# Kernel optimization log

Measured on AMD Instinct MI355X. Metric: run time of the kernel, lower is better.

Reference implementation:

```python
import jax, jax.numpy as jnp
import numpy as np

B, NA, NB = 2, 2048, 2048
DIM_A, DIM_B = 256, 256
HEADS, DH_A, DH_B = 8, 64, 64
INNER_A, INNER_B = DH_A * HEADS, DH_B * HEADS
EPS = 1e-5


def layer_norm(x, w, b):
    m = jnp.mean(x, axis=-1, keepdims=True)
    v = jnp.mean(jnp.square(x - m), axis=-1, keepdims=True)
    return (x - m) * jax.lax.rsqrt(v + EPS) * w + b


def setup_inputs() -> dict:
    key = jax.random.key(0)
    ks = jax.random.split(key, 16)
    s = 0.02
    return {
        "feat_a": jax.random.normal(ks[0], (B, NA, DIM_A), jnp.float32),
        "feat_b": jax.random.normal(ks[1], (B, NB, DIM_B), jnp.float32),
        "mask_a_b": jax.random.bernoulli(ks[2], 0.5, (B, NA, NB)),
        # linear weights stored (in, out)
        "Wq": jax.random.normal(ks[3], (DIM_A, INNER_B), jnp.float32) * s,
        "bq": jnp.zeros((INNER_B,), jnp.float32),
        "Wk": jax.random.normal(ks[4], (DIM_B, INNER_B), jnp.float32) * s,
        "bk": jnp.zeros((INNER_B,), jnp.float32),
        "Wv": jax.random.normal(ks[5], (DIM_B, INNER_A), jnp.float32) * s,
        "bv": jnp.zeros((INNER_A,), jnp.float32),
        "Wg": jax.random.normal(ks[6], (DIM_A, INNER_A), jnp.float32) * s,
        "bg": jnp.zeros((INNER_A,), jnp.float32),
        "Wo": jax.random.normal(ks[7], (INNER_A, DIM_A), jnp.float32) * s,
        "bo": jnp.zeros((DIM_A,), jnp.float32),
        "ln_a_w": jnp.ones((DIM_A,), jnp.float32),
        "ln_a_b": jnp.zeros((DIM_A,), jnp.float32),
        "ln_b_w": jnp.ones((DIM_B,), jnp.float32),
        "ln_b_b": jnp.zeros((DIM_B,), jnp.float32),
        "qln_w": jnp.ones((INNER_B,), jnp.float32),
        "qln_b": jnp.zeros((INNER_B,), jnp.float32),
        "kln_w": jnp.ones((INNER_B,), jnp.float32),
        "kln_b": jnp.zeros((INNER_B,), jnp.float32),
    }


def reference(feat_a, feat_b, mask_a_b, Wq, bq, Wk, bk, Wv, bv, Wg, bg, Wo, bo,
              ln_a_w, ln_a_b, ln_b_w, ln_b_b, qln_w, qln_b, kln_w, kln_b):
    scale = DH_B ** -0.5
    fa = layer_norm(feat_a, ln_a_w, ln_a_b)            # (b, na, dim_a)
    fb = layer_norm(feat_b, ln_b_w, ln_b_b)            # (b, nb, dim_b)
    q = layer_norm(fa @ Wq + bq, qln_w, qln_b)         # (b, na, inner_b)
    k = layer_norm(fb @ Wk + bk, kln_w, kln_b)         # (b, nb, inner_b)
    v = fb @ Wv + bv                                   # (b, nb, inner_a)
    g = fa @ Wg + bg                                   # (b, na, inner_a)
    q = q.reshape(B, NA, HEADS, DH_B)
    k = k.reshape(B, NB, HEADS, DH_B)
    v = v.reshape(B, NB, HEADS, DH_A)
    g = g.reshape(B, NA, HEADS, DH_A)
    sim = jnp.einsum('bihd,bjhd->bhij', q, k) * scale  # (b, h, na, nb)
    neg = jnp.finfo(sim.dtype).min
    sim = jnp.where(mask_a_b[:, None, :, :], sim, neg)
    attn = jax.nn.softmax(sim, axis=-1)
    out = jnp.einsum('bhij,bjhd->bihd', attn, v)       # (b, na, h, dh_a)
    out = jax.nn.sigmoid(g) * out
    out = out.reshape(B, NA, INNER_A)
    return out @ Wo + bo                               # (b, na, dim_a)
```

## Files before the change

kernel.cpp:

```cpp
#include <hip/hip_runtime.h>
#include <hip/hip_bf16.h>

using bf16 = __hip_bfloat16;
typedef short bf16x8 __attribute__((ext_vector_type(8)));
typedef float f32x4 __attribute__((ext_vector_type(4)));
typedef unsigned short ushort8_t __attribute__((ext_vector_type(8)));
typedef unsigned uint4_t __attribute__((ext_vector_type(4)));
typedef unsigned long long u64;

static constexpr int NA_ = 2048, NB_ = 2048;
static constexpr int H_ = 8, DH_ = 64, INNER_ = 512;
static constexpr int MROWS = 2 * NA_;

#define MFMA32(a, b, c) __builtin_amdgcn_mfma_f32_16x16x32_bf16(a, b, c, 0, 0, 0)

#if __has_builtin(__builtin_amdgcn_exp2f)
#define EXP2(x) __builtin_amdgcn_exp2f(x)
#else
#define EXP2(x) exp2f(x)
#endif

__device__ __forceinline__ unsigned short bfbits(float x) {
  bf16 h = __float2bfloat16(x);
  return __builtin_bit_cast(unsigned short, h);
}
__device__ __forceinline__ float b2f(unsigned short u) {
  unsigned v = ((unsigned)u) << 16;
  return __builtin_bit_cast(float, v);
}

__device__ __forceinline__ unsigned pkbf(float a, float b) {
  unsigned ua = __builtin_bit_cast(unsigned, a) + 0x8000u;
  unsigned ub = __builtin_bit_cast(unsigned, b) + 0x8000u;
#if __has_builtin(__builtin_amdgcn_perm)
  return __builtin_amdgcn_perm(ub, ua, 0x07060302u);
#else
  return (ua >> 16) | (ub & 0xFFFF0000u);
#endif
}

__global__ __launch_bounds__(256) void prep_kernel(
    const float* __restrict__ fa_in, const float* __restrict__ fb_in,
    const float* __restrict__ law, const float* __restrict__ lab,
    const float* __restrict__ lbw, const float* __restrict__ lbb,
    bf16* __restrict__ fa, bf16* __restrict__ fb,
    const float* __restrict__ Wq, const float* __restrict__ Wk,
    const float* __restrict__ Wv, const float* __restrict__ Wg,
    const float* __restrict__ Wo,
    bf16* __restrict__ Wqt, bf16* __restrict__ Wkt,
    bf16* __restrict__ Wvt, bf16* __restrict__ Wgt,
    bf16* __restrict__ Woth, bf16* __restrict__ Wotl,
    const void* __restrict__ maskp, u64* __restrict__ mbits) {
  int blk = blockIdx.x;
  int t = threadIdx.x;
  if (blk < 2048) {
    int row = blk * 4 + (t >> 6);
    int lane = t & 63;
    const float *src, *w, *bb;
    bf16* dst;
    int r;
    if (row < MROWS) { src = fa_in; w = law; bb = lab; dst = fa; r = row; }
    else             { src = fb_in; w = lbw; bb = lbb; dst = fb; r = row - MROWS; }
    float4 x = *(const float4*)(src + (size_t)r * 256 + lane * 4);
    float s  = (x.x + x.y) + (x.z + x.w);
    float s2 = (x.x * x.x + x.y * x.y) + (x.z * x.z + x.w * x.w);
#pragma unroll
    for (int m = 32; m >= 1; m >>= 1) { s += __shfl_xor(s, m); s2 += __shfl_xor(s2, m); }
    float mean = s * (1.0f / 256.0f);
    float var  = s2 * (1.0f / 256.0f) - mean * mean;
    float rstd = rsqrtf(var + 1e-5f);
    float4 wv = *(const float4*)(w + lane * 4);
    float4 bv = *(const float4*)(bb + lane * 4);
    ushort4 o;
    o.x = bfbits((x.x - mean) * rstd * wv.x + bv.x);
    o.y = bfbits((x.y - mean) * rstd * wv.y + bv.y);
    o.z = bfbits((x.z - mean) * rstd * wv.z + bv.z);
    o.w = bfbits((x.w - mean) * rstd * wv.w + bv.w);
    *(ushort4*)(dst + (size_t)r * 256 + lane * 4) = o;
  } else if (blk < 4608) {
    int z = (blk - 2048) >> 9;
    int idx = ((blk - 2048) & 511) * 256 + t;
    if (z < 4) {
      const float* W = (z == 0) ? Wq : (z == 1) ? Wk : (z == 2) ? Wv : Wg;
      bf16* Wt = (z == 0) ? Wqt : (z == 1) ? Wkt : (z == 2) ? Wvt : Wgt;
      int kk = idx >> 9, n = idx & 511;
      Wt[n * 256 + kk] = __float2bfloat16(W[idx]);
    } else {
      int kk = idx >> 8, n = idx & 255;
      float w = Wo[idx];
      bf16 hi = __float2bfloat16(w);
      Woth[n * 512 + kk] = hi;
      Wotl[n * 512 + kk] = __float2bfloat16(w - __bfloat162float(hi));
    }
  } else {
    __shared__ unsigned shf[4];
    const unsigned char* mu = (const unsigned char*)maskp;
    bool nz = ((t & 3) != 0) && (mu[t] != 0);
    u64 bal = __ballot(nz);
    if ((t & 63) == 0) shf[t >> 6] = (bal != 0ull) ? 1u : 0u;
    __syncthreads();
    bool m8 = (shf[0] | shf[1] | shf[2] | shf[3]) != 0;
    int lane = t & 63, wid = t >> 6;
    int lb = blk - 4608;
    for (size_t word = (size_t)lb * 4 + wid; word < 131072; word += 8192) {
      size_t e = word * 64 + lane;
      int v = m8 ? (int)mu[e] : ((const int*)maskp)[e];
      u64 b2 = __ballot(v != 0);
      if (lane == 0) mbits[word] = b2;
    }
  }
}

__global__ __launch_bounds__(256) void gemm4_kernel(
    const bf16* __restrict__ fa, const bf16* __restrict__ fb,
    const bf16* __restrict__ Wqt, const bf16* __restrict__ Wkt,
    const bf16* __restrict__ Wgt, const bf16* __restrict__ Wvt,
    const float* __restrict__ bq, const float* __restrict__ bk,
    const float* __restrict__ bg, const float* __restrict__ bv,
    const float* __restrict__ qlw, const float* __restrict__ qlb,
    const float* __restrict__ klw, const float* __restrict__ klb,
    bf16* __restrict__ qo, bf16* __restrict__ ko,
    bf16* __restrict__ gout, bf16* __restrict__ vout) {
  __shared__ __align__(16) char sm[27648];
  int z = blockIdx.z;
  int t = threadIdx.x, wave = t >> 6, lane = t & 63;
  int lm = lane & 15, quad = lane >> 4, q8 = quad * 8;

  if (z < 2) {
    bf16* As = (bf16*)sm;
    float* Pred = (float*)(sm + 16896);
    float* MV   = (float*)(sm + 17408);
    const bf16* A    = z ? fb : fa;
    const bf16* Wt   = z ? Wkt : Wqt;
    const float* bias = z ? bk : bq;
    const float* lw  = z ? klw : qlw;
    const float* lb  = z ? klb : qlb;
    bf16* out        = z ? ko : qo;
    int m0 = blockIdx.x * 16;
#pragma unroll
    for (int i = 0; i < 2; i++) {
      int id = t + 256 * i, r = id >> 5, cg = id & 31;
      *(ushort8_t*)(&As[r * 264 + cg * 8]) =
          *(const ushort8_t*)(A + (size_t)(m0 + r) * 256 + cg * 8);
    }
    __syncthreads();
    int n0w = wave * 128;
    f32x4 acc[8] = {};
    const bf16* wrow[8];
#pragma unroll
    for (int ni = 0; ni < 8; ni++) wrow[ni] = Wt + (size_t)(n0w + ni * 16 + lm) * 256;
#pragma unroll
    for (int ks = 0; ks < 8; ks++) {
      int k0 = ks * 32;
      bf16x8 af = *(const bf16x8*)(&As[lm * 264 + k0 + q8]);
#pragma unroll
      for (int ni = 0; ni < 8; ni++) {
        bf16x8 bf_ = *(const bf16x8*)(wrow[ni] + k0 + q8);
        acc[ni] = MFMA32(af, bf_, acc[ni]);
      }
    }
    float bvv[8];
#pragma unroll
    for (int ni = 0; ni < 8; ni++) bvv[ni] = bias[n0w + ni * 16 + lm];
#pragma unroll
    for (int ni = 0; ni < 8; ni++)
#pragma unroll
      for (int r = 0; r < 4; r++) acc[ni][r] += bvv[ni];
#pragma unroll
    for (int r = 0; r < 4; r++) {
      float s = 0.f, s2 = 0.f;
#pragma unroll
      for (int ni = 0; ni < 8; ni++) { s += acc[ni][r]; s2 += acc[ni][r] * acc[ni][r]; }
#pragma unroll
      for (int m = 1; m <= 8; m <<= 1) { s += __shfl_xor(s, m); s2 += __shfl_xor(s2, m); }
      if (lm == 0) {
        int row = quad * 4 + r;
        Pred[row * 8 + wave * 2]     = s;
        Pred[row * 8 + wave * 2 + 1] = s2;
      }
    }
    __syncthreads();
    if (t < 16) {
      float s = 0.f, s2 = 0.f;
#pragma unroll
      for (int w = 0; w < 4; w++) { s += Pred[t * 8 + w * 2]; s2 += Pred[t * 8 + w * 2 + 1]; }
      float mean = s * (1.0f / 512.0f);
      float var  = s2 * (1.0f / 512.0f) - mean * mean;
      MV[t * 2]     = mean;
      MV[t * 2 + 1] = rsqrtf(var + 1e-5f);
    }
    __syncthreads();
    float lww[8], lbb_[8];
#pragma unroll
    for (int ni = 0; ni < 8; ni++) {
      lww[ni]  = lw[n0w + ni * 16 + lm];
      lbb_[ni] = lb[n0w + ni * 16 + lm];
    }
    if (z == 0) {
      const float SC = 0.125f * 1.44269504088896f;
#pragma unroll
      for (int ni = 0; ni < 8; ni++) { lww[ni] *= SC; lbb_[ni] *= SC; }
    }
#pragma unroll
    for (int r = 0; r < 4; r++) {
      int row = quad * 4 + r;
      float mean = MV[row * 2], rstd = MV[row * 2 + 1];
      size_t obase = (size_t)(m0 + row) * 512 + n0w;
#pragma unroll
      for (int ni = 0; ni < 8; ni++)
        out[obase + ni * 16 + lm] =
            __float2bfloat16((acc[ni][r] - mean) * rstd * lww[ni] + lbb_[ni]);
    }
  } else {
    bf16* As = (bf16*)sm;
    bf16* Bs = (bf16*)(sm + 18432);
    const bf16* A    = (z == 3) ? fb : fa;
    const bf16* Wt   = (z == 3) ? Wvt : Wgt;
    const float* bias = (z == 3) ? bv : bg;
    int x = blockIdx.x;
    int m0 = (x >> 3) * 128, n0 = (x & 7) * 64;
    int wm = wave * 32;
    f32x4 acc[2][4] = {};
    for (int k0 = 0; k0 < 256; k0 += 64) {
      __syncthreads();
#pragma unroll
      for (int i = 0; i < 4; i++) {
        int id = t + 256 * i, r = id >> 3, cg = id & 7;
        *(ushort8_t*)(&As[r * 72 + cg * 8]) =
            *(const ushort8_t*)(A + (size_t)(m0 + r) * 256 + k0 + cg * 8);
      }
#pragma unroll
      for (int i = 0; i < 2; i++) {
        int id = t + 256 * i, r = id >> 3, cg = id & 7;
        *(ushort8_t*)(&Bs[r * 72 + cg * 8]) =
            *(const ushort8_t*)(Wt + (size_t)(n0 + r) * 256 + k0 + cg * 8);
      }
      __syncthreads();
#pragma unroll
      for (int kk = 0; kk < 64; kk += 32) {
        bf16x8 af[2], bf_[4];
#pragma unroll
        for (int mi = 0; mi < 2; mi++)
          af[mi] = *(const bf16x8*)(&As[(wm + mi * 16 + lm) * 72 + kk + q8]);
#pragma unroll
        for (int ni = 0; ni < 4; ni++)
          bf_[ni] = *(const bf16x8*)(&Bs[(ni * 16 + lm) * 72 + kk + q8]);
#pragma unroll
        for (int mi = 0; mi < 2; mi++)
#pragma unroll
          for (int ni = 0; ni < 4; ni++)
            acc[mi][ni] = MFMA32(af[mi], bf_[ni], acc[mi][ni]);
      }
    }
    if (z == 2) {
#pragma unroll
      for (int mi = 0; mi < 2; mi++)
#pragma unroll
        for (int ni = 0; ni < 4; ni++) {
          int nn = n0 + ni * 16 + lm;
          float bvv = bias[nn];
          int mb = m0 + wm + mi * 16 + quad * 4;
#pragma unroll
          for (int r = 0; r < 4; r++)
            gout[(size_t)(mb + r) * 512 + nn] = __float2bfloat16(acc[mi][ni][r] + bvv);
        }
    } else {
      __syncthreads();
      bf16* buf = (bf16*)sm;
#pragma unroll
      for (int mi = 0; mi < 2; mi++)
#pragma unroll
        for (int ni = 0; ni < 4; ni++) {
          int d_local = ni * 16 + lm;
          float bvv = bias[n0 + d_local];
          int j_local = wm + mi * 16 + quad * 4;
#pragma unroll
          for (int r = 0; r < 4; r++)
            buf[d_local * 136 + j_local + r] = __float2bfloat16(acc[mi][ni][r] + bvv);
        }
      __syncthreads();
      int bidx2 = m0 >> 11, j0g = m0 & 2047, hh = n0 >> 6;
      int dl = t >> 2, jseg = (t & 3) * 32;
      bf16* dstrow = vout + (size_t)((bidx2 * 8 + hh) * 64 + dl) * 2048 + j0g + jseg;
#pragma unroll
      for (int c = 0; c < 4; c++)
        *(ushort8_t*)(dstrow + c * 8) = *(const ushort8_t*)(&buf[dl * 136 + jseg + c * 8]);
    }
  }
}

__global__ __launch_bounds__(512, 6) void attn_kernel(
    const bf16* __restrict__ q, const bf16* __restrict__ k,
    const bf16* __restrict__ vt, const bf16* __restrict__ g,
    const u64* __restrict__ mbits,
    bf16* __restrict__ gh, bf16* __restrict__ gl) {
  __shared__ __align__(16) char smem[46592];
  bf16* Qs = (bf16*)smem;
  bf16* KsB = (bf16*)(smem + 9216);
  bf16* VsB = (bf16*)(smem + 27648);
  float* Om = (float*)(smem + 9216);
  float* Lbuf = (float*)(smem + 46080);

  int qt = blockIdx.x, bh = blockIdx.y;
  int bidx = bh >> 3, h = bh & 7;
  int i0 = qt * 64;
  int t = threadIdx.x, wave = t >> 6, lane = t & 63;
  int jhalf = wave >> 2, w4 = wave & 3;
  int lm = lane & 15, quad = lane >> 4, q8 = quad * 8;
  int lt = t & 255;
  int sr0 = lt >> 3, scg = (lt & 7) * 8;

  int ksrow = ((sr0 & 4) << 2) | ((sr0 & 24) >> 1) | (sr0 & 3);
  int ksl0 = ksrow * 72 + scg;
  int ksl1 = (ksrow + 32) * 72 + scg;
  int vsl0 = sr0 * 72 + scg;
  int vsl1 = (sr0 + 32) * 72 + scg;

  {
    int r = t >> 3, cg = t & 7;
    *(ushort8_t*)(&Qs[r * 72 + cg * 8]) =
        *(const ushort8_t*)(q + (size_t)(bidx * NA_ + i0 + r) * INNER_ + h * DH_ + cg * 8);
  }
  __syncthreads();
  bf16x8 bq0 = *(const bf16x8*)(&Qs[(w4 * 16 + lm) * 72 + q8]);
  bf16x8 bq1 = *(const bf16x8*)(&Qs[(w4 * 16 + lm) * 72 + 32 + q8]);

  bf16x8 bone;
  {
    short onev = (lm == 0) ? (short)0x3F80 : (short)0;
#pragma unroll
    for (int i = 0; i < 8; i++) bone[i] = onev;
  }

  f32x4 oacc[4] = {};
  f32x4 lacc = {};

  const bf16* kb = k + (size_t)(bidx * NB_) * INNER_ + h * DH_;
  const bf16* vb = vt + (size_t)(bh * DH_) * NB_;
  bf16* Ks = KsB + jhalf * (64 * 72);
  bf16* Vs = VsB + jhalf * (64 * 72);
  const u64* mrp = mbits + ((size_t)(bidx * NA_ + i0 + w4 * 16 + lm)) * (NB_ / 64) + jhalf * 16;

  const bf16* ksrc0 = kb + (size_t)(jhalf * 1024 + sr0) * INNER_ + scg;
  const bf16* ksrc1 = kb + (size_t)(jhalf * 1024 + sr0 + 32) * INNER_ + scg;
  const bf16* vsrc0 = vb + (size_t)sr0 * NB_ + jhalf * 1024 + scg;
  const bf16* vsrc1 = vb + (size_t)(sr0 + 32) * NB_ + jhalf * 1024 + scg;

  ushort8_t kr0, kr1, vr0, vr1;
  kr0 = *(const ushort8_t*)(ksrc0);
  kr1 = *(const ushort8_t*)(ksrc1);
  vr0 = *(const ushort8_t*)(vsrc0);
  vr1 = *(const ushort8_t*)(vsrc1);
  u64 smw = mrp[0] >> (quad * 8);

  for (int it = 0; it < 16; it++) {
    __syncthreads();
    *(ushort8_t*)(&Ks[ksl0]) = kr0;
    *(ushort8_t*)(&Ks[ksl1]) = kr1;
    *(ushort8_t*)(&Vs[vsl0]) = vr0;
    *(ushort8_t*)(&Vs[vsl1]) = vr1;
    __syncthreads();

    u64 nsm = smw;
    if (it < 15) {
      int joff = (it + 1) * 64;
      kr0 = *(const ushort8_t*)(ksrc0 + (size_t)joff * INNER_);
      kr1 = *(const ushort8_t*)(ksrc1 + (size_t)joff * INNER_);
      vr0 = *(const ushort8_t*)(vsrc0 + joff);
      vr1 = *(const ushort8_t*)(vsrc1 + joff);
      nsm = mrp[it + 1] >> (quad * 8);
    }

    f32x4 st[4];
#pragma unroll
    for (int nt = 0; nt < 4; nt++) {
      bf16x8 a0 = *(const bf16x8*)(&Ks[(nt * 16 + lm) * 72 + q8]);
      bf16x8 a1 = *(const bf16x8*)(&Ks[(nt * 16 + lm) * 72 + 32 + q8]);
      f32x4 a = {0.f, 0.f, 0.f, 0.f};
      a = MFMA32(a0, bq0, a);
      a = MFMA32(a1, bq1, a);
      st[nt] = a;
    }

    float pr[4][4];
#pragma unroll
    for (int nt = 0; nt < 4; nt++)
#pragma unroll
      for (int r = 0; r < 4; r++) {
        int bitix = (nt >> 1) * 32 + (nt & 1) * 4 + r;
        bool live = (smw >> bitix) & 1ull;
        float sv = live ? st[nt][r] : -200.0f;
        pr[nt][r] = EXP2(sv);
      }

    uint4_t ua, ub;
    ua[0] = pkbf(pr[0][0], pr[0][1]);
    ua[1] = pkbf(pr[0][2], pr[0][3]);
    ua[2] = pkbf(pr[1][0], pr[1][1]);
    ua[3] = pkbf(pr[1][2], pr[1][3]);
    ub[0] = pkbf(pr[2][0], pr[2][1]);
    ub[1] = pkbf(pr[2][2], pr[2][3]);
    ub[2] = pkbf(pr[3][0], pr[3][1]);
    ub[3] = pkbf(pr[3][2], pr[3][3]);
    bf16x8 ap0 = __builtin_bit_cast(bf16x8, ua);
    bf16x8 ap1 = __builtin_bit_cast(bf16x8, ub);

#pragma unroll
    for (int c = 0; c < 4; c++) {
      bf16x8 v0 = *(const bf16x8*)(&Vs[(c * 16 + lm) * 72 + q8]);
      bf16x8 v1 = *(const bf16x8*)(&Vs[(c * 16 + lm) * 72 + 32 + q8]);
      oacc[c] = MFMA32(ap0, v0, oacc[c]);
      oacc[c] = MFMA32(ap1, v1, oacc[c]);
    }
    lacc = MFMA32(ap0, bone, lacc);
    lacc = MFMA32(ap1, bone, lacc);

    smw = nsm;
  }

  __syncthreads();
  if (lm == 0) {
#pragma unroll
    for (int r = 0; r < 4; r++)
      Lbuf[jhalf * 64 + w4 * 16 + quad * 4 + r] = lacc[r];
  }
  if (jhalf == 1) {
#pragma unroll
    for (int c = 0; c < 4; c++)
#pragma unroll
      for (int r = 0; r < 4; r++)
        Om[w4 * (16 * 66) + (quad * 4 + r) * 66 + c * 16 + lm] = oacc[c][r];
  }
  __syncthreads();
  if (jhalf == 0) {
    int mrow = i0 + w4 * 16 + quad * 4;
    float inv[4];
#pragma unroll
    for (int r = 0; r < 4; r++) {
      float l = Lbuf[w4 * 16 + quad * 4 + r] + Lbuf[64 + w4 * 16 + quad * 4 + r];
      inv[r] = 1.0f / l;
    }
#pragma unroll
    for (int c = 0; c < 4; c++) {
      int col = h * DH_ + c * 16 + lm;
#pragma unroll
      for (int r = 0; r < 4; r++) {
        float o = oacc[c][r] + Om[w4 * (16 * 66) + (quad * 4 + r) * 66 + c * 16 + lm];
        size_t idx = (size_t)(bidx * NA_ + mrow + r) * INNER_ + col;
        float gv = b2f(__builtin_bit_cast(unsigned short, g[idx]));
        float sig = 1.0f / (1.0f + __expf(-gv));
        float val = o * inv[r] * sig;
        unsigned short hb = bfbits(val);
        gh[idx] = __builtin_bit_cast(bf16, hb);
        gl[idx] = __float2bfloat16(val - b2f(hb));
      }
    }
  }
}

__global__ __launch_bounds__(256) void gemm_split_kernel(
    const bf16* __restrict__ Ah, const bf16* __restrict__ Al,
    const bf16* __restrict__ Bh, const bf16* __restrict__ Bl,
    const float* __restrict__ bias, float* __restrict__ C) {
  constexpr int K = 512, N = 256;
  __shared__ __align__(16) bf16 Ash[32 * 72];
  __shared__ __align__(16) bf16 Asl[32 * 72];
  __shared__ __align__(16) bf16 Bsh[64 * 72];
  __shared__ __align__(16) bf16 Bsl[64 * 72];
  int n0 = blockIdx.x * 64, m0 = blockIdx.y * 32;
  int t = threadIdx.x, wave = t >> 6, lane = t & 63;
  int lm = lane & 15, quad = lane >> 4, q8 = quad * 8;
  int wm = (wave & 1) * 16, wn = (wave >> 1) * 32;
  f32x4 acc[2] = {};
  for (int k0 = 0; k0 < K; k0 += 64) {
    __syncthreads();
    {
      int r = t >> 3, cg = t & 7;
      size_t ga = (size_t)(m0 + r) * K + k0 + cg * 8;
      *(ushort8_t*)(&Ash[r * 72 + cg * 8]) = *(const ushort8_t*)(Ah + ga);
      *(ushort8_t*)(&Asl[r * 72 + cg * 8]) = *(const ushort8_t*)(Al + ga);
    }
#pragma unroll
    for (int i = 0; i < 2; i++) {
      int id = t + 256 * i, r = id >> 3, cg = id & 7;
      size_t gb = (size_t)(n0 + r) * K + k0 + cg * 8;
      *(ushort8_t*)(&Bsh[r * 72 + cg * 8]) = *(const ushort8_t*)(Bh + gb);
      *(ushort8_t*)(&Bsl[r * 72 + cg * 8]) = *(const ushort8_t*)(Bl + gb);
    }
    __syncthreads();
#pragma unroll
    for (int kk = 0; kk < 64; kk += 32) {
      bf16x8 ah = *(const bf16x8*)(&Ash[(wm + lm) * 72 + kk + q8]);
      bf16x8 al = *(const bf16x8*)(&Asl[(wm + lm) * 72 + kk + q8]);
#pragma unroll
      for (int ni = 0; ni < 2; ni++) {
        bf16x8 bh_ = *(const bf16x8*)(&Bsh[(wn + ni * 16 + lm) * 72 + kk + q8]);
        bf16x8 bl_ = *(const bf16x8*)(&Bsl[(wn + ni * 16 + lm) * 72 + kk + q8]);
        acc[ni] = MFMA32(ah, bh_, acc[ni]);
        acc[ni] = MFMA32(ah, bl_, acc[ni]);
        acc[ni] = MFMA32(al, bh_, acc[ni]);
      }
    }
  }
#pragma unroll
  for (int ni = 0; ni < 2; ni++) {
    int n = n0 + wn + ni * 16 + lm;
    float bvv = bias[n];
    int mb = m0 + wm + quad * 4;
#pragma unroll
    for (int r = 0; r < 4; r++) C[(size_t)(mb + r) * N + n] = acc[ni][r] + bvv;
  }
}

extern "C" void kernel_launch(void* const* d_in, const int* in_sizes, int n_in,
                              void* d_out, int out_size, void* d_ws, size_t ws_size,
                              hipStream_t stream) {
  const float* feat_a = (const float*)d_in[0];
  const float* feat_b = (const float*)d_in[1];
  const void*  mask   = d_in[2];
  const float* Wq = (const float*)d_in[3];
  const float* bq = (const float*)d_in[4];
  const float* Wk = (const float*)d_in[5];
  const float* bk = (const float*)d_in[6];
  const float* Wv = (const float*)d_in[7];
  const float* bv = (const float*)d_in[8];
  const float* Wg = (const float*)d_in[9];
  const float* bg = (const float*)d_in[10];
  const float* Wo = (const float*)d_in[11];
  const float* bo = (const float*)d_in[12];
  const float* law = (const float*)d_in[13];
  const float* lab = (const float*)d_in[14];
  const float* lbw = (const float*)d_in[15];
  const float* lbb = (const float*)d_in[16];
  const float* qlw = (const float*)d_in[17];
  const float* qlb = (const float*)d_in[18];
  const float* klw = (const float*)d_in[19];
  const float* klb = (const float*)d_in[20];

  char* ws = (char*)d_ws;
  size_t off = 0;
  auto alloc = [&](size_t bytes) -> void* {
    void* p = ws + off;
    off += (bytes + 255) & ~(size_t)255;
    return p;
  };
  bf16* fa    = (bf16*)alloc((size_t)MROWS * 256 * 2);
  bf16* fb    = (bf16*)alloc((size_t)MROWS * 256 * 2);
  bf16* Wqt   = (bf16*)alloc((size_t)131072 * 2);
  bf16* Wkt   = (bf16*)alloc((size_t)131072 * 2);
  bf16* Wvt   = (bf16*)alloc((size_t)131072 * 2);
  bf16* Wgt   = (bf16*)alloc((size_t)131072 * 2);
  bf16* Woth  = (bf16*)alloc((size_t)131072 * 2);
  bf16* Wotl  = (bf16*)alloc((size_t)131072 * 2);
  bf16* qb_   = (bf16*)alloc((size_t)MROWS * 512 * 2);
  bf16* kb_   = (bf16*)alloc((size_t)MROWS * 512 * 2);
  bf16* vtb   = (bf16*)alloc((size_t)1024 * 2048 * 2);
  bf16* gbuf  = (bf16*)alloc((size_t)MROWS * 512 * 2);
  bf16* gh    = (bf16*)alloc((size_t)MROWS * 512 * 2);
  bf16* gl    = (bf16*)alloc((size_t)MROWS * 512 * 2);
  u64*  mbits = (u64*)alloc((size_t)131072 * 8);

  prep_kernel<<<6656, 256, 0, stream>>>(
      feat_a, feat_b, law, lab, lbw, lbb, fa, fb,
      Wq, Wk, Wv, Wg, Wo, Wqt, Wkt, Wvt, Wgt, Woth, Wotl, mask, mbits);
  gemm4_kernel<<<dim3(256, 1, 4), 256, 0, stream>>>(
      fa, fb, Wqt, Wkt, Wgt, Wvt, bq, bk, bg, bv,
      qlw, qlb, klw, klb, qb_, kb_, gbuf, vtb);
  attn_kernel<<<dim3(32, 16), 512, 0, stream>>>(qb_, kb_, vtb, gbuf, mbits, gh, gl);
  gemm_split_kernel<<<dim3(4, 128), 256, 0, stream>>>(gh, gl, Woth, Wotl, bo, (float*)d_out);
}
```

Baseline: 195.1 us.

## Retile attention waves into 2x2 query/key sub-blocks with four-way partial reduction

Each wave now computes a 32x32 query-by-key score tile instead of a 16x64 strip, so every K fragment is reused across two query row groups and every V fragment read from shared memory feeds two accumulators. This cuts LDS reads per MFMA. In exchange each wave holds twice the output accumulators and per-row sums, so the launch bound drops from 6 to 4 waves per SIMD. The epilogue becomes a four-way reduction through shared memory with extra barriers, and the Lbuf region grows to hold four partial row sums.

```diff
diff --git a/kernel.cpp b/kernel.cpp
--- a/kernel.cpp
+++ b/kernel.cpp
@@ -289,12 +289,12 @@
   }
 }
 
-__global__ __launch_bounds__(512, 6) void attn_kernel(
+__global__ __launch_bounds__(512, 4) void attn_kernel(
     const bf16* __restrict__ q, const bf16* __restrict__ k,
     const bf16* __restrict__ vt, const bf16* __restrict__ g,
     const u64* __restrict__ mbits,
     bf16* __restrict__ gh, bf16* __restrict__ gl) {
-  __shared__ __align__(16) char smem[46592];
+  __shared__ __align__(16) char smem[47104];
   bf16* Qs = (bf16*)smem;
   bf16* KsB = (bf16*)(smem + 9216);
   bf16* VsB = (bf16*)(smem + 27648);
@@ -305,8 +305,9 @@
   int bidx = bh >> 3, h = bh & 7;
   int i0 = qt * 64;
   int t = threadIdx.x, wave = t >> 6, lane = t & 63;
-  int jhalf = wave >> 2, w4 = wave & 3;
+  int jh = wave >> 2, wj = (wave >> 1) & 1, wi = wave & 1;
   int lm = lane & 15, quad = lane >> 4, q8 = quad * 8;
+  int wj32 = wj * 32, wi32 = wi * 32;
   int lt = t & 255;
   int sr0 = lt >> 3, scg = (lt & 7) * 8;
 
@@ -322,8 +323,10 @@
         *(const ushort8_t*)(q + (size_t)(bidx * NA_ + i0 + r) * INNER_ + h * DH_ + cg * 8);
   }
   __syncthreads();
-  bf16x8 bq0 = *(const bf16x8*)(&Qs[(w4 * 16 + lm) * 72 + q8]);
-  bf16x8 bq1 = *(const bf16x8*)(&Qs[(w4 * 16 + lm) * 72 + 32 + q8]);
+  bf16x8 bq00 = *(const bf16x8*)(&Qs[(wi32 + lm) * 72 + q8]);
+  bf16x8 bq01 = *(const bf16x8*)(&Qs[(wi32 + lm) * 72 + 32 + q8]);
+  bf16x8 bq10 = *(const bf16x8*)(&Qs[(wi32 + 16 + lm) * 72 + q8]);
+  bf16x8 bq11 = *(const bf16x8*)(&Qs[(wi32 + 16 + lm) * 72 + 32 + q8]);
 
   bf16x8 bone;
   {
@@ -332,26 +335,29 @@
     for (int i = 0; i < 8; i++) bone[i] = onev;
   }
 
-  f32x4 oacc[4] = {};
-  f32x4 lacc = {};
+  f32x4 oacc[2][4] = {};
+  f32x4 lacc[2] = {};
 
   const bf16* kb = k + (size_t)(bidx * NB_) * INNER_ + h * DH_;
   const bf16* vb = vt + (size_t)(bh * DH_) * NB_;
-  bf16* Ks = KsB + jhalf * (64 * 72);
-  bf16* Vs = VsB + jhalf * (64 * 72);
-  const u64* mrp = mbits + ((size_t)(bidx * NA_ + i0 + w4 * 16 + lm)) * (NB_ / 64) + jhalf * 16;
-
-  const bf16* ksrc0 = kb + (size_t)(jhalf * 1024 + sr0) * INNER_ + scg;
-  const bf16* ksrc1 = kb + (size_t)(jhalf * 1024 + sr0 + 32) * INNER_ + scg;
-  const bf16* vsrc0 = vb + (size_t)sr0 * NB_ + jhalf * 1024 + scg;
-  const bf16* vsrc1 = vb + (size_t)(sr0 + 32) * NB_ + jhalf * 1024 + scg;
+  bf16* Ks = KsB + jh * (64 * 72);
+  bf16* Vs = VsB + jh * (64 * 72);
+  const u64* mrp0 = mbits + ((size_t)(bidx * NA_ + i0 + wi32 + lm)) * (NB_ / 64) + jh * 16;
+  const u64* mrp1 = mrp0 + 16 * (NB_ / 64);
+  int shp = wj32 + quad * 8;
+
+  const bf16* ksrc0 = kb + (size_t)(jh * 1024 + sr0) * INNER_ + scg;
+  const bf16* ksrc1 = kb + (size_t)(jh * 1024 + sr0 + 32) * INNER_ + scg;
+  const bf16* vsrc0 = vb + (size_t)sr0 * NB_ + jh * 1024 + scg;
+  const bf16* vsrc1 = vb + (size_t)(sr0 + 32) * NB_ + jh * 1024 + scg;
 
   ushort8_t kr0, kr1, vr0, vr1;
   kr0 = *(const ushort8_t*)(ksrc0);
   kr1 = *(const ushort8_t*)(ksrc1);
   vr0 = *(const ushort8_t*)(vsrc0);
   vr1 = *(const ushort8_t*)(vsrc1);
-  u64 smw = mrp[0] >> (quad * 8);
+  u64 smw0 = mrp0[0] >> shp;
+  u64 smw1 = mrp1[0] >> shp;
 
   for (int it = 0; it < 16; it++) {
     __syncthreads();
@@ -361,98 +367,135 @@
     *(ushort8_t*)(&Vs[vsl1]) = vr1;
     __syncthreads();
 
-    u64 nsm = smw;
+    u64 n0m = smw0, n1m = smw1;
     if (it < 15) {
       int joff = (it + 1) * 64;
       kr0 = *(const ushort8_t*)(ksrc0 + (size_t)joff * INNER_);
       kr1 = *(const ushort8_t*)(ksrc1 + (size_t)joff * INNER_);
       vr0 = *(const ushort8_t*)(vsrc0 + joff);
       vr1 = *(const ushort8_t*)(vsrc1 + joff);
-      nsm = mrp[it + 1] >> (quad * 8);
-    }
-
-    f32x4 st[4];
-#pragma unroll
-    for (int nt = 0; nt < 4; nt++) {
-      bf16x8 a0 = *(const bf16x8*)(&Ks[(nt * 16 + lm) * 72 + q8]);
-      bf16x8 a1 = *(const bf16x8*)(&Ks[(nt * 16 + lm) * 72 + 32 + q8]);
-      f32x4 a = {0.f, 0.f, 0.f, 0.f};
-      a = MFMA32(a0, bq0, a);
-      a = MFMA32(a1, bq1, a);
-      st[nt] = a;
-    }
-
-    float pr[4][4];
-#pragma unroll
-    for (int nt = 0; nt < 4; nt++)
-#pragma unroll
-      for (int r = 0; r < 4; r++) {
-        int bitix = (nt >> 1) * 32 + (nt & 1) * 4 + r;
-        bool live = (smw >> bitix) & 1ull;
-        float sv = live ? st[nt][r] : -200.0f;
-        pr[nt][r] = EXP2(sv);
-      }
-
-    uint4_t ua, ub;
-    ua[0] = pkbf(pr[0][0], pr[0][1]);
-    ua[1] = pkbf(pr[0][2], pr[0][3]);
-    ua[2] = pkbf(pr[1][0], pr[1][1]);
-    ua[3] = pkbf(pr[1][2], pr[1][3]);
-    ub[0] = pkbf(pr[2][0], pr[2][1]);
-    ub[1] = pkbf(pr[2][2], pr[2][3]);
-    ub[2] = pkbf(pr[3][0], pr[3][1]);
-    ub[3] = pkbf(pr[3][2], pr[3][3]);
-    bf16x8 ap0 = __builtin_bit_cast(bf16x8, ua);
-    bf16x8 ap1 = __builtin_bit_cast(bf16x8, ub);
+      n0m = mrp0[it + 1] >> shp;
+      n1m = mrp1[it + 1] >> shp;
+    }
+
+    bf16x8 a00 = *(const bf16x8*)(&Ks[(wj32 + lm) * 72 + q8]);
+    bf16x8 a01 = *(const bf16x8*)(&Ks[(wj32 + lm) * 72 + 32 + q8]);
+    bf16x8 a10 = *(const bf16x8*)(&Ks[(wj32 + 16 + lm) * 72 + q8]);
+    bf16x8 a11 = *(const bf16x8*)(&Ks[(wj32 + 16 + lm) * 72 + 32 + q8]);
+    f32x4 st[2][2];
+    {
+      f32x4 x;
+      x = f32x4{0.f, 0.f, 0.f, 0.f};
+      x = MFMA32(a00, bq00, x); x = MFMA32(a01, bq01, x); st[0][0] = x;
+      x = f32x4{0.f, 0.f, 0.f, 0.f};
+      x = MFMA32(a10, bq00, x); x = MFMA32(a11, bq01, x); st[0][1] = x;
+      x = f32x4{0.f, 0.f, 0.f, 0.f};
+      x = MFMA32(a00, bq10, x); x = MFMA32(a01, bq11, x); st[1][0] = x;
+      x = f32x4{0.f, 0.f, 0.f, 0.f};
+      x = MFMA32(a10, bq10, x); x = MFMA32(a11, bq11, x); st[1][1] = x;
+    }
+
+#pragma unroll
+    for (int is_ = 0; is_ < 2; is_++) {
+      u64 w = is_ ? smw1 : smw0;
+#pragma unroll
+      for (int js = 0; js < 2; js++)
+#pragma unroll
+        for (int r = 0; r < 4; r++) {
+          bool live = (w >> (js * 4 + r)) & 1ull;
+          float sv = live ? st[is_][js][r] : -200.0f;
+          st[is_][js][r] = EXP2(sv);
+        }
+    }
+
+    uint4_t u0, u1;
+    u0[0] = pkbf(st[0][0][0], st[0][0][1]);
+    u0[1] = pkbf(st[0][0][2], st[0][0][3]);
+    u0[2] = pkbf(st[0][1][0], st[0][1][1]);
+    u0[3] = pkbf(st[0][1][2], st[0][1][3]);
+    u1[0] = pkbf(st[1][0][0], st[1][0][1]);
+    u1[1] = pkbf(st[1][0][2], st[1][0][3]);
+    u1[2] = pkbf(st[1][1][0], st[1][1][1]);
+    u1[3] = pkbf(st[1][1][2], st[1][1][3]);
+    bf16x8 pa0 = __builtin_bit_cast(bf16x8, u0);
+    bf16x8 pa1 = __builtin_bit_cast(bf16x8, u1);
 
 #pragma unroll
     for (int c = 0; c < 4; c++) {
-      bf16x8 v0 = *(const bf16x8*)(&Vs[(c * 16 + lm) * 72 + q8]);
-      bf16x8 v1 = *(const bf16x8*)(&Vs[(c * 16 + lm) * 72 + 32 + q8]);
-      oacc[c] = MFMA32(ap0, v0, oacc[c]);
-      oacc[c] = MFMA32(ap1, v1, oacc[c]);
-    }
-    lacc = MFMA32(ap0, bone, lacc);
-    lacc = MFMA32(ap1, bone, lacc);
-
-    smw = nsm;
+      bf16x8 v_ = *(const bf16x8*)(&Vs[(c * 16 + lm) * 72 + wj32 + q8]);
+      oacc[0][c] = MFMA32(pa0, v_, oacc[0][c]);
+      oacc[1][c] = MFMA32(pa1, v_, oacc[1][c]);
+    }
+    lacc[0] = MFMA32(pa0, bone, lacc[0]);
+    lacc[1] = MFMA32(pa1, bone, lacc[1]);
+
+    smw0 = n0m;
+    smw1 = n1m;
   }
 
   __syncthreads();
   if (lm == 0) {
 #pragma unroll
-    for (int r = 0; r < 4; r++)
-      Lbuf[jhalf * 64 + w4 * 16 + quad * 4 + r] = lacc[r];
-  }
-  if (jhalf == 1) {
-#pragma unroll
-    for (int c = 0; c < 4; c++)
+    for (int is_ = 0; is_ < 2; is_++)
 #pragma unroll
       for (int r = 0; r < 4; r++)
-        Om[w4 * (16 * 66) + (quad * 4 + r) * 66 + c * 16 + lm] = oacc[c][r];
+        Lbuf[(jh * 2 + wj) * 64 + wi32 + is_ * 16 + quad * 4 + r] = lacc[is_][r];
+  }
+  if (jh == 1 && wj == 1) {
+#pragma unroll
+    for (int is_ = 0; is_ < 2; is_++)
+#pragma unroll
+      for (int c = 0; c < 4; c++)
+#pragma unroll
+        for (int r = 0; r < 4; r++)
+          Om[(wi32 + is_ * 16 + quad * 4 + r) * 66 + c * 16 + lm] = oacc[is_][c][r];
   }
   __syncthreads();
-  if (jhalf == 0) {
-    int mrow = i0 + w4 * 16 + quad * 4;
-    float inv[4];
-#pragma unroll
-    for (int r = 0; r < 4; r++) {
-      float l = Lbuf[w4 * 16 + quad * 4 + r] + Lbuf[64 + w4 * 16 + quad * 4 + r];
-      inv[r] = 1.0f / l;
-    }
-#pragma unroll
-    for (int c = 0; c < 4; c++) {
-      int col = h * DH_ + c * 16 + lm;
+  if (jh == 1 && wj == 0) {
+#pragma unroll
+    for (int is_ = 0; is_ < 2; is_++)
+#pragma unroll
+      for (int c = 0; c < 4; c++)
+#pragma unroll
+        for (int r = 0; r < 4; r++)
+          Om[(wi32 + is_ * 16 + quad * 4 + r) * 66 + c * 16 + lm] += oacc[is_][c][r];
+  }
+  __syncthreads();
+  if (jh == 0 && wj == 1) {
+#pragma unroll
+    for (int is_ = 0; is_ < 2; is_++)
+#pragma unroll
+      for (int c = 0; c < 4; c++)
+#pragma unroll
+        for (int r = 0; r < 4; r++)
+          Om[(wi32 + is_ * 16 + quad * 4 + r) * 66 + c * 16 + lm] += oacc[is_][c][r];
+  }
+  __syncthreads();
+  if (jh == 0 && wj == 0) {
+#pragma unroll
+    for (int is_ = 0; is_ < 2; is_++) {
+      int ib = wi32 + is_ * 16 + quad * 4;
+      float inv[4];
 #pragma unroll
       for (int r = 0; r < 4; r++) {
-        float o = oacc[c][r] + Om[w4 * (16 * 66) + (quad * 4 + r) * 66 + c * 16 + lm];
-        size_t idx = (size_t)(bidx * NA_ + mrow + r) * INNER_ + col;
-        float gv = b2f(__builtin_bit_cast(unsigned short, g[idx]));
-        float sig = 1.0f / (1.0f + __expf(-gv));
-        float val = o * inv[r] * sig;
-        unsigned short hb = bfbits(val);
-        gh[idx] = __builtin_bit_cast(bf16, hb);
-        gl[idx] = __float2bfloat16(val - b2f(hb));
+        int il = ib + r;
+        float l = Lbuf[il] + Lbuf[64 + il] + Lbuf[128 + il] + Lbuf[192 + il];
+        inv[r] = 1.0f / l;
+      }
+#pragma unroll
+      for (int c = 0; c < 4; c++) {
+        int col = h * DH_ + c * 16 + lm;
+#pragma unroll
+        for (int r = 0; r < 4; r++) {
+          float o = oacc[is_][c][r] + Om[(ib + r) * 66 + c * 16 + lm];
+          size_t idx = (size_t)(bidx * NA_ + i0 + ib + r) * INNER_ + col;
+          float gv = b2f(__builtin_bit_cast(unsigned short, g[idx]));
+          float sig = 1.0f / (1.0f + __expf(-gv));
+          float val = o * inv[r] * sig;
+          unsigned short hb = bfbits(val);
+          gh[idx] = __builtin_bit_cast(bf16, hb);
+          gl[idx] = __float2bfloat16(val - b2f(hb));
+        }
       }
     }
   }
```

Measured after the change: 194.9 us. No clear change (-0.1%).
